# Kernel optimization log

Measured on AMD Instinct MI355X. Metric: run time of the kernel, lower is better.

The kernel has to match this reference:

```python
import jax, jax.numpy as jnp
import numpy as np

N = 100000      # nodes
E = 1600000     # edges
F = 92          # raw node feature length
H = 128         # element_embedding == hidden_encoding (GatedGraphConv out_channels)
STEPS = 6       # mpnn_steps
G = 256         # graphs in batch


def setup_inputs() -> dict:
    key = jax.random.key(0)
    ks = jax.random.split(key, 10)
    s = 0.05
    x = jax.random.normal(ks[0], (N, F), dtype=jnp.float32)
    edge_index = jax.random.randint(ks[1], (2, E), 0, N, dtype=jnp.int64)
    batch = jnp.sort(jax.random.randint(ks[2], (N,), 0, G, dtype=jnp.int64))
    # atom_input: Linear(F, H, bias=False); applied as x @ W_embed with W_embed [F, H]
    W_embed = jax.random.normal(ks[3], (F, H), dtype=jnp.float32) * s
    # GatedGraphConv weight: [num_layers, H, H], used as h @ W_mpnn[i]
    W_mpnn = jax.random.normal(ks[4], (STEPS, H, H), dtype=jnp.float32) * s
    # torch.nn.GRUCell params: weight_ih/hh [3H, H], bias_ih/hh [3H]
    w_ih = jax.random.normal(ks[5], (3 * H, H), dtype=jnp.float32) * s
    w_hh = jax.random.normal(ks[6], (3 * H, H), dtype=jnp.float32) * s
    b_ih = jax.random.normal(ks[7], (3 * H,), dtype=jnp.float32) * s
    b_hh = jax.random.normal(ks[8], (3 * H,), dtype=jnp.float32) * s
    # prediction_layer: Linear(H, 1)
    w_pred = jax.random.normal(ks[9], (H, 1), dtype=jnp.float32) * s
    b_pred = jnp.zeros((1,), dtype=jnp.float32)
    return {"x": x, "edge_index": edge_index, "batch": batch,
            "W_embed": W_embed, "W_mpnn": W_mpnn,
            "w_ih": w_ih, "w_hh": w_hh, "b_ih": b_ih, "b_hh": b_hh,
            "w_pred": w_pred, "b_pred": b_pred}


def reference(x, edge_index, batch, W_embed, W_mpnn, w_ih, w_hh, b_ih, b_hh, w_pred, b_pred):
    n = x.shape[0]
    src, dst = edge_index[0], edge_index[1]  # PyG: messages flow source -> target
    # atom_input (no bias) + tanh; element_embedding == H so no zero-padding needed
    h = jnp.tanh(x @ W_embed)  # [N, H]

    def step(h, W):
        m = h @ W                                             # per-step linear [N, H]
        agg = jax.ops.segment_sum(m[src], dst, num_segments=n)  # scatter-add aggr
        # torch GRUCell(input=agg, hidden=h)
        gi = agg @ w_ih.T + b_ih                              # [N, 3H]
        gh = h @ w_hh.T + b_hh                                # [N, 3H]
        i_r, i_z, i_n = jnp.split(gi, 3, axis=-1)
        h_r, h_z, h_n = jnp.split(gh, 3, axis=-1)
        r = jax.nn.sigmoid(i_r + h_r)
        z = jax.nn.sigmoid(i_z + h_z)
        cand = jnp.tanh(i_n + r * h_n)
        h_new = (1.0 - z) * cand + z * h
        return h_new, None

    h, _ = jax.lax.scan(step, h, W_mpnn)

    # global_mean_pool over graph ids
    sums = jax.ops.segment_sum(h, batch, num_segments=G)                           # [G, H]
    counts = jax.ops.segment_sum(jnp.ones((n, 1), h.dtype), batch, num_segments=G)  # [G, 1]
    pooled = sums / jnp.maximum(counts, 1.0)
    pooled = jax.nn.relu(pooled)
    return (pooled @ w_pred + b_pred)[:, 0]  # [G]
```

## Files before the change

### kernel.cpp

```cpp
#include <hip/hip_runtime.h>
#include <math.h>

#define N_NODES 100000
#define N_PAD   100032
#define N_EDGES 1600000
#define F_IN    92
#define H_DIM   128
#define STEPS   6
#define G_GRAPHS 256
#define TH3     384
#define SSTR    136
#define HSTR    132
#define FPASS   8
#define FRANGE  12500
#define EIDX_CAP 1024

typedef __attribute__((ext_vector_type(8))) short bf16x8;
typedef __attribute__((ext_vector_type(4))) float f32x4;

__device__ __forceinline__ unsigned short f2bf(float x) {
    unsigned u = __float_as_uint(x);
    return (unsigned short)((u + 0x7fffu + ((u >> 16) & 1u)) >> 16);
}
__device__ __forceinline__ float bf2f(unsigned short h) {
    return __uint_as_float(((unsigned)h) << 16);
}

__global__ void fuse_w_kernel(const float* __restrict__ Wm, const float* __restrict__ w_ih,
                              float* __restrict__ M2) {
    int ij = blockIdx.x;
    int i  = ij / TH3;
    int j  = ij - i * TH3;
    int k  = threadIdx.x;
    __shared__ float wj[H_DIM];
    wj[k] = w_ih[j * H_DIM + k];
    __syncthreads();
    const float* wr = Wm + ((size_t)i * H_DIM + k) * H_DIM;
    float acc = 0.f;
    #pragma unroll 4
    for (int c = 0; c < H_DIM; ++c) acc = fmaf(wj[c], wr[c], acc);
    M2[((size_t)i * TH3 + j) * H_DIM + k] = acc;
}

__global__ void pack_kernel(const float* __restrict__ M6, const float* __restrict__ w_hh,
                            unsigned short* __restrict__ PBhi, unsigned short* __restrict__ PBlo) {
    int b    = blockIdx.x;
    int lane = threadIdx.x;
    int kc   = b & 3;
    int ct   = (b >> 2) & 7;
    int mg   = b >> 5;
    int g    = mg % 3;
    int mat  = mg / 3;
    int j    = g * 128 + ct * 16 + (lane & 15);
    int k0   = kc * 32 + (lane >> 4) * 8;
    size_t outBase = ((size_t)b * 64 + lane) * 8;
    #pragma unroll
    for (int jj = 0; jj < 8; ++jj) {
        int k = k0 + jj;
        float v = (mat < 6) ? M6[((size_t)mat * TH3 + j) * H_DIM + k]
                            : w_hh[(size_t)j * H_DIM + k];
        unsigned short hv = f2bf(v);
        PBhi[outBase + jj] = hv;
        PBlo[outBase + jj] = f2bf(v - bf2f(hv));
    }
}

#define ET 16
__global__ void embed_kernel(const float* __restrict__ x, const float* __restrict__ We,
                             unsigned short* __restrict__ h_hi, unsigned short* __restrict__ h_lo) {
    int n0 = blockIdx.x * ET;
    int j  = threadIdx.x;
    __shared__ float xs[ET * F_IN];
    for (int i = j; i < ET * F_IN; i += H_DIM) xs[i] = x[n0 * F_IN + i];
    __syncthreads();
    float acc[ET];
    #pragma unroll
    for (int n = 0; n < ET; ++n) acc[n] = 0.f;
    const float4* xs4 = (const float4*)xs;
    for (int k4 = 0; k4 < F_IN / 4; ++k4) {
        int k = k4 * 4;
        float w0 = We[(k + 0) * H_DIM + j];
        float w1 = We[(k + 1) * H_DIM + j];
        float w2 = We[(k + 2) * H_DIM + j];
        float w3 = We[(k + 3) * H_DIM + j];
        #pragma unroll
        for (int n = 0; n < ET; ++n) {
            float4 a = xs4[n * (F_IN / 4) + k4];
            acc[n] = fmaf(a.x, w0, acc[n]);
            acc[n] = fmaf(a.y, w1, acc[n]);
            acc[n] = fmaf(a.z, w2, acc[n]);
            acc[n] = fmaf(a.w, w3, acc[n]);
        }
    }
    #pragma unroll
    for (int n = 0; n < ET; ++n) {
        float e2 = __expf(2.f * acc[n]);
        float v  = 1.f - 2.f / (e2 + 1.f);
        size_t o = (size_t)(n0 + n) * H_DIM + j;
        unsigned short hv = f2bf(v);
        h_hi[o] = hv;
        h_lo[o] = f2bf(v - bf2f(hv));
    }
}

__global__ void hist_kernel(const int* __restrict__ dst, int* __restrict__ count) {
    int e = blockIdx.x * 256 + threadIdx.x;
    if (e < N_EDGES) atomicAdd(&count[dst[e]], 1);
}

__global__ void scan_block_kernel(const int* __restrict__ count, int* __restrict__ offs,
                                  int* __restrict__ blockSums) {
    __shared__ int tmp[256];
    int i = blockIdx.x * 256 + threadIdx.x;
    int t = threadIdx.x;
    int v = (i < N_NODES) ? count[i] : 0;
    tmp[t] = v;
    __syncthreads();
    for (int d = 1; d < 256; d <<= 1) {
        int add = (t >= d) ? tmp[t - d] : 0;
        __syncthreads();
        tmp[t] += add;
        __syncthreads();
    }
    if (i < N_NODES) offs[i] = tmp[t] - v;
    if (t == 255) blockSums[blockIdx.x] = tmp[255];
}

__global__ void scan_sums_kernel(int* __restrict__ blockSums, int nb) {
    __shared__ int tmp[512];
    int t = threadIdx.x;
    int v = (t < nb) ? blockSums[t] : 0;
    tmp[t] = v;
    __syncthreads();
    for (int d = 1; d < 512; d <<= 1) {
        int add = (t >= d) ? tmp[t - d] : 0;
        __syncthreads();
        tmp[t] += add;
        __syncthreads();
    }
    if (t < nb) blockSums[t] = tmp[t] - v;
}

__global__ void scan_add_kernel(int* __restrict__ offs, const int* __restrict__ blockSums) {
    int i = blockIdx.x * 256 + threadIdx.x;
    if (i < N_NODES) offs[i] += blockSums[blockIdx.x];
    if (i == 0) offs[N_NODES] = N_EDGES;
}

__global__ void fill_kernel(const int* __restrict__ src, const int* __restrict__ dst,
                            const int* __restrict__ offs, int* __restrict__ cursor,
                            int* __restrict__ srcSorted) {
    int e = blockIdx.x * 256 + threadIdx.x;
    if (e >= N_EDGES) return;
    for (int p = 0; p < FPASS; ++p) {
        int lo = p * FRANGE;
        int d = dst[e];
        if (d >= lo && d < lo + FRANGE) {
            int pos = atomicAdd(&cursor[d], 1);
            srcSorted[offs[d] + pos] = src[e];
        }
    }
}

__global__ __launch_bounds__(512, 4) void gru_fused_kernel(
    const unsigned short* __restrict__ h_hi_in,
    unsigned short* __restrict__ h_hi_out,
    unsigned short* __restrict__ h_lo,
    const int* __restrict__ offs, const int* __restrict__ srcS,
    const unsigned short* __restrict__ PBhi, const unsigned short* __restrict__ PBlo,
    int matI, const float* __restrict__ b_ih, const float* __restrict__ b_hh)
{
    __shared__ __align__(16) unsigned short buf[3 * 32 * SSTR];
    __shared__ int eIdx[EIDX_CAP];
    unsigned short* sHh = buf;
    unsigned short* sHl = buf + 32 * SSTR;
    unsigned short* sS  = buf + 2 * 32 * SSTR;
    float* hnF = (float*)buf;

    int nt = blockIdx.x;
    int rowBase = nt * 32;
    int t = threadIdx.x;
    int row = t >> 4;
    int node = rowBase + row;

    int beg = 0, end = 0;
    if (node < N_NODES) { beg = offs[node]; end = offs[node + 1]; }
    int eBegBlk = offs[rowBase < N_NODES ? rowBase : N_NODES];
    int eEndBlk = offs[(rowBase + 32) < N_NODES ? (rowBase + 32) : N_NODES];
    int eCnt = eEndBlk - eBegBlk;

    {
        int c8 = (t & 15) * 8;
        size_t g = (size_t)node * H_DIM + c8;
        int l = row * SSTR + c8;
        *(bf16x8*)&sHh[l] = *(const bf16x8*)(h_hi_in + g);
        *(bf16x8*)&sHl[l] = *(const bf16x8*)(h_lo + g);
    }
    {
        int lim = eCnt < EIDX_CAP ? eCnt : EIDX_CAP;
        for (int k = t; k < lim; k += 512) eIdx[k] = srcS[eBegBlk + k];
    }
    __syncthreads();

    {
        int sub   = t & 15;
        int halfI = sub >> 3;
        int cOff  = (sub & 7) * 16;
        float a[16];
        #pragma unroll
        for (int j = 0; j < 16; ++j) a[j] = 0.f;
        if (node < N_NODES) {
            int len = end - beg;
            int h0  = (len + 1) >> 1;
            int lo  = beg + (halfI ? h0 : 0);
            int hi  = halfI ? end : beg + h0;
            const unsigned short* hb = h_hi_in + cOff;

            auto gatherRun = [&](auto IDXF) {
                int i = lo;
                int n0 = 0, n1 = 0, n2 = 0, n3 = 0;
                bool have4 = (i + 4 <= hi);
                if (have4) { n0 = IDXF(i); n1 = IDXF(i+1); n2 = IDXF(i+2); n3 = IDXF(i+3); }
                while (have4) {
                    const bf16x8* p0 = (const bf16x8*)(hb + (size_t)n0 * H_DIM);
                    const bf16x8* p1 = (const bf16x8*)(hb + (size_t)n1 * H_DIM);
                    const bf16x8* p2 = (const bf16x8*)(hb + (size_t)n2 * H_DIM);
                    const bf16x8* p3 = (const bf16x8*)(hb + (size_t)n3 * H_DIM);
                    bf16x8 v0a = p0[0], v0b = p0[1];
                    bf16x8 v1a = p1[0], v1b = p1[1];
                    bf16x8 v2a = p2[0], v2b = p2[1];
                    bf16x8 v3a = p3[0], v3b = p3[1];
                    i += 4;
                    have4 = (i + 4 <= hi);
                    if (have4) { n0 = IDXF(i); n1 = IDXF(i+1); n2 = IDXF(i+2); n3 = IDXF(i+3); }
                    #pragma unroll
                    for (int j = 0; j < 8; ++j) {
                        a[j]     += (bf2f((unsigned short)v0a[j]) + bf2f((unsigned short)v1a[j]))
                                  + (bf2f((unsigned short)v2a[j]) + bf2f((unsigned short)v3a[j]));
                        a[8 + j] += (bf2f((unsigned short)v0b[j]) + bf2f((unsigned short)v1b[j]))
                                  + (bf2f((unsigned short)v2b[j]) + bf2f((unsigned short)v3b[j]));
                    }
                }
                if (i + 2 <= hi) {
                    int q0 = IDXF(i), q1 = IDXF(i + 1);
                    const bf16x8* p0 = (const bf16x8*)(hb + (size_t)q0 * H_DIM);
                    const bf16x8* p1 = (const bf16x8*)(hb + (size_t)q1 * H_DIM);
                    bf16x8 v0a = p0[0], v0b = p0[1];
                    bf16x8 v1a = p1[0], v1b = p1[1];
                    #pragma unroll
                    for (int j = 0; j < 8; ++j) {
                        a[j]     += bf2f((unsigned short)v0a[j]) + bf2f((unsigned short)v1a[j]);
                        a[8 + j] += bf2f((unsigned short)v0b[j]) + bf2f((unsigned short)v1b[j]);
                    }
                    i += 2;
                }
                if (i < hi) {
                    int q0 = IDXF(i);
                    const bf16x8* p = (const bf16x8*)(hb + (size_t)q0 * H_DIM);
                    bf16x8 va = p[0], vb = p[1];
                    #pragma unroll
                    for (int j = 0; j < 8; ++j) {
                        a[j]     += bf2f((unsigned short)va[j]);
                        a[8 + j] += bf2f((unsigned short)vb[j]);
                    }
                }
            };

            if (eCnt <= EIDX_CAP) {
                int eb = eBegBlk;
                gatherRun([&](int x) { return eIdx[x - eb]; });
            } else {
                gatherRun([&](int x) { return srcS[x]; });
            }
        }
        #pragma unroll
        for (int j = 0; j < 16; ++j) a[j] += __shfl_xor(a[j], 8);
        bf16x8 o;
        #pragma unroll
        for (int j = 0; j < 8; ++j) o[j] = (short)f2bf(a[halfI * 8 + j]);
        *(bf16x8*)&sS[row * SSTR + cOff + halfI * 8] = o;
    }

    int lane = t & 63;
    int ct   = t >> 6;
    int rloc = lane & 15;
    int kOff = (lane >> 4) * 8;

    f32x4 accRZ[2][2], accIn[2], accHn[2];
    #pragma unroll
    for (int rs = 0; rs < 2; ++rs) {
        accRZ[0][rs] = (f32x4){0.f, 0.f, 0.f, 0.f};
        accRZ[1][rs] = (f32x4){0.f, 0.f, 0.f, 0.f};
        accIn[rs]    = (f32x4){0.f, 0.f, 0.f, 0.f};
        accHn[rs]    = (f32x4){0.f, 0.f, 0.f, 0.f};
    }

    for (int kc = 0; kc < 4; ++kc) {
        int aOff = kc * 32 + kOff;
        bf16x8 aHh4[2], aHl4[2];
        #pragma unroll
        for (int rs = 0; rs < 2; ++rs) {
            int al = (rs * 16 + rloc) * SSTR + aOff;
            aHh4[rs] = *(const bf16x8*)(&sHh[al]);
            aHl4[rs] = *(const bf16x8*)(&sHl[al]);
        }
        #pragma unroll
        for (int g = 0; g < 3; ++g) {
            size_t oH = ((size_t)((18 + g) * 32 + ct * 4 + kc) * 64 + lane) * 8;
            bf16x8 bHh = *(const bf16x8*)(PBhi + oH);
            bf16x8 bHl = *(const bf16x8*)(PBlo + oH);
            #pragma unroll
            for (int rs = 0; rs < 2; ++rs) {
                f32x4* tH = (g == 0) ? &accRZ[0][rs] : (g == 1) ? &accRZ[1][rs] : &accHn[rs];
                *tH = __builtin_amdgcn_mfma_f32_16x16x32_bf16(aHh4[rs], bHh, *tH, 0, 0, 0);
                *tH = __builtin_amdgcn_mfma_f32_16x16x32_bf16(aHl4[rs], bHh, *tH, 0, 0, 0);
                *tH = __builtin_amdgcn_mfma_f32_16x16x32_bf16(aHh4[rs], bHl, *tH, 0, 0, 0);
            }
        }
    }

    __syncthreads();

    const int fI0 = matI * 3;
    for (int kc = 0; kc < 4; ++kc) {
        int aOff = kc * 32 + kOff;
        bf16x8 aS[2];
        #pragma unroll
        for (int rs = 0; rs < 2; ++rs)
            aS[rs] = *(const bf16x8*)(&sS[(rs * 16 + rloc) * SSTR + aOff]);
        #pragma unroll
        for (int g = 0; g < 3; ++g) {
            size_t oI = ((size_t)((fI0 + g) * 32 + ct * 4 + kc) * 64 + lane) * 8;
            bf16x8 bIh = *(const bf16x8*)(PBhi + oI);
            bf16x8 bIl = *(const bf16x8*)(PBlo + oI);
            #pragma unroll
            for (int rs = 0; rs < 2; ++rs) {
                f32x4* tI = (g == 0) ? &accRZ[0][rs] : (g == 1) ? &accRZ[1][rs] : &accIn[rs];
                *tI = __builtin_amdgcn_mfma_f32_16x16x32_bf16(aS[rs], bIh, *tI, 0, 0, 0);
                *tI = __builtin_amdgcn_mfma_f32_16x16x32_bf16(aS[rs], bIl, *tI, 0, 0, 0);
            }
        }
    }

    int c = ct * 16 + rloc;
    float br  = b_ih[c] + b_hh[c];
    float bz  = b_ih[128 + c] + b_hh[128 + c];
    float bin = b_ih[256 + c], bhn = b_hh[256 + c];
    int rl = (lane >> 4) * 4;

    float hnv[2][4];
    #pragma unroll
    for (int rs = 0; rs < 2; ++rs) {
        #pragma unroll
        for (int r = 0; r < 4; ++r) {
            int lrow = rs * 16 + rl + r;
            float hold = bf2f(sHh[lrow * SSTR + c]) + bf2f(sHl[lrow * SSTR + c]);
            float rr = 1.f / (1.f + __expf(-(accRZ[0][rs][r] + br)));
            float zz = 1.f / (1.f + __expf(-(accRZ[1][rs][r] + bz)));
            float pre = (accIn[rs][r] + bin) + rr * (accHn[rs][r] + bhn);
            float e2 = __expf(2.f * pre);
            float cand = 1.f - 2.f / (e2 + 1.f);
            hnv[rs][r] = (1.f - zz) * cand + zz * hold;
        }
    }
    __syncthreads();
    #pragma unroll
    for (int rs = 0; rs < 2; ++rs)
        #pragma unroll
        for (int r = 0; r < 4; ++r)
            hnF[(rs * 16 + rl + r) * HSTR + c] = hnv[rs][r];
    __syncthreads();
    #pragma unroll
    for (int i = t; i < 32 * 32; i += 512) {
        int rw = i >> 5;
        int c4 = (i & 31) * 4;
        int gRow = rowBase + rw;
        if (gRow < N_NODES) {
            float4 v = *(const float4*)(&hnF[rw * HSTR + c4]);
            ushort4 hh, ll;
            hh.x = f2bf(v.x); ll.x = f2bf(v.x - bf2f(hh.x));
            hh.y = f2bf(v.y); ll.y = f2bf(v.y - bf2f(hh.y));
            hh.z = f2bf(v.z); ll.z = f2bf(v.z - bf2f(hh.z));
            hh.w = f2bf(v.w); ll.w = f2bf(v.w - bf2f(hh.w));
            size_t o = (size_t)gRow * H_DIM + c4;
            *(ushort4*)(h_hi_out + o) = hh;
            *(ushort4*)(h_lo + o) = ll;
        }
    }
}

__global__ void pool_partial(const unsigned short* __restrict__ h_hi,
                             const unsigned short* __restrict__ h_lo,
                             const int* __restrict__ batch,
                             float* __restrict__ pooled) {
    int b = blockIdx.x;
    int t = threadIdx.x;
    int n0 = b * 64;
    if (n0 >= N_NODES) return;
    int nEnd = n0 + 64 < N_NODES ? n0 + 64 : N_NODES;
    int curG = batch[n0];
    float acc = 0.f;
    for (int n = n0; n < nEnd; ++n) {
        int g = batch[n];
        if (g != curG) {
            atomicAdd(&pooled[curG * H_DIM + t], acc);
            acc = 0.f;
            curG = g;
        }
        size_t o = (size_t)n * H_DIM + t;
        acc += bf2f(h_hi[o]) + bf2f(h_lo[o]);
    }
    atomicAdd(&pooled[curG * H_DIM + t], acc);
}

__global__ void pool_head(const float* __restrict__ pooled, const int* __restrict__ batch,
                          const float* __restrict__ w_pred, const float* __restrict__ b_pred,
                          float* __restrict__ out) {
    int g = blockIdx.x;
    int t = threadIdx.x;
    __shared__ int bounds[2];
    __shared__ float red[2];
    if (t < 2) {
        int target = g + t;
        int lo = 0, hi = N_NODES;
        while (lo < hi) {
            int mid = (lo + hi) >> 1;
            if (batch[mid] < target) lo = mid + 1; else hi = mid;
        }
        bounds[t] = lo;
    }
    __syncthreads();
    int cnt = bounds[1] - bounds[0];
    float pv = pooled[g * H_DIM + t] / fmaxf((float)cnt, 1.f);
    pv = fmaxf(pv, 0.f);
    float v = pv * w_pred[t];
    #pragma unroll
    for (int off = 32; off > 0; off >>= 1) v += __shfl_down(v, off);
    if ((t & 63) == 0) red[t >> 6] = v;
    __syncthreads();
    if (t == 0) out[g] = red[0] + red[1] + b_pred[0];
}

extern "C" void kernel_launch(void* const* d_in, const int* in_sizes, int n_in,
                              void* d_out, int out_size, void* d_ws, size_t ws_size,
                              hipStream_t stream) {
    const float* x      = (const float*)d_in[0];
    const int*   ei     = (const int*)d_in[1];
    const int*   batch  = (const int*)d_in[2];
    const float* We     = (const float*)d_in[3];
    const float* Wm     = (const float*)d_in[4];
    const float* w_ih   = (const float*)d_in[5];
    const float* w_hh   = (const float*)d_in[6];
    const float* b_ih   = (const float*)d_in[7];
    const float* b_hh   = (const float*)d_in[8];
    const float* w_pred = (const float*)d_in[9];
    const float* b_pred = (const float*)d_in[10];
    float* out = (float*)d_out;

    const size_t HN = (size_t)N_PAD * H_DIM;
    unsigned short* h_hiA = (unsigned short*)d_ws;
    unsigned short* h_lo  = h_hiA + HN;
    unsigned short* h_hiB = h_lo + HN;
    float* M6 = (float*)(h_hiB + HN);
    unsigned short* PBhi = (unsigned short*)(M6 + (size_t)STEPS * TH3 * H_DIM);
    unsigned short* PBlo = PBhi + 21 * 32 * 64 * 8;
    int* offs      = (int*)(PBlo + 21 * 32 * 64 * 8);
    int* srcSorted = offs + (N_NODES + 1);
    float* pooled  = (float*)(srcSorted + N_EDGES);
    int* count     = (int*)h_hiB;
    int* cursor    = count + N_NODES;
    int* blockSums = cursor + N_NODES;

    const int* esrc = ei;
    const int* edst = ei + N_EDGES;
    const int EB = (N_EDGES + 255) / 256;
    const int NB = (N_NODES + 255) / 256;

    hipMemsetAsync(count, 0, 2 * (size_t)N_NODES * sizeof(int), stream);
    hipMemsetAsync(pooled, 0, (size_t)G_GRAPHS * H_DIM * sizeof(float), stream);
    hist_kernel<<<EB, 256, 0, stream>>>(edst, count);
    scan_block_kernel<<<NB, 256, 0, stream>>>(count, offs, blockSums);
    scan_sums_kernel<<<1, 512, 0, stream>>>(blockSums, NB);
    scan_add_kernel<<<NB, 256, 0, stream>>>(offs, blockSums);
    fill_kernel<<<EB, 256, 0, stream>>>(esrc, edst, offs, cursor, srcSorted);

    fuse_w_kernel<<<STEPS * TH3, H_DIM, 0, stream>>>(Wm, w_ih, M6);
    pack_kernel<<<21 * 32, 64, 0, stream>>>(M6, w_hh, PBhi, PBlo);
    embed_kernel<<<N_NODES / ET, H_DIM, 0, stream>>>(x, We, h_hiA, h_lo);

    for (int i = 0; i < STEPS; ++i) {
        const unsigned short* hin = (i & 1) ? h_hiB : h_hiA;
        unsigned short*       hout = (i & 1) ? h_hiA : h_hiB;
        gru_fused_kernel<<<N_PAD / 32, 512, 0, stream>>>(hin, hout, h_lo,
                                                         offs, srcSorted, PBhi, PBlo,
                                                         i, b_ih, b_hh);
    }

    pool_partial<<<(N_NODES + 63) / 64, H_DIM, 0, stream>>>(h_hiA, h_lo, batch, pooled);
    pool_head<<<G_GRAPHS, H_DIM, 0, stream>>>(pooled, batch, w_pred, b_pred, out);
}
```

Before: 1.045 ms.

## Tile fuse_w over output rows and alternate gather/MFMA order across blocks

The weight-fusion kernel now has each block compute eight output rows at once, loading w_ih rows into shared memory and reading Wm with float4 loads. This cuts the block count and reuses each Wm row load. In the GRU step kernel, the neighbour gather and the hidden-state MFMA phase become lambdas whose order flips based on a thread/block-derived parity. The aim is to mix memory-bound and compute-bound wavefronts on a CU so they overlap better. The catch is extra register pressure from keeping the accumulators live across the gather, and the gathered sS is only consumed after the barrier.

```diff
diff --git a/kernel.cpp b/kernel.cpp
--- a/kernel.cpp
+++ b/kernel.cpp
@@ -14,6 +14,7 @@
 #define FPASS   8
 #define FRANGE  12500
 #define EIDX_CAP 1024
+#define JT      8
 
 typedef __attribute__((ext_vector_type(8))) short bf16x8;
 typedef __attribute__((ext_vector_type(4))) float f32x4;
@@ -29,17 +30,33 @@
 __global__ void fuse_w_kernel(const float* __restrict__ Wm, const float* __restrict__ w_ih,
                               float* __restrict__ M2) {
     int ij = blockIdx.x;
-    int i  = ij / TH3;
-    int j  = ij - i * TH3;
+    int i  = ij / (TH3 / JT);
+    int j0 = (ij % (TH3 / JT)) * JT;
     int k  = threadIdx.x;
-    __shared__ float wj[H_DIM];
-    wj[k] = w_ih[j * H_DIM + k];
-    __syncthreads();
-    const float* wr = Wm + ((size_t)i * H_DIM + k) * H_DIM;
-    float acc = 0.f;
-    #pragma unroll 4
-    for (int c = 0; c < H_DIM; ++c) acc = fmaf(wj[c], wr[c], acc);
-    M2[((size_t)i * TH3 + j) * H_DIM + k] = acc;
+    __shared__ float wj[JT][H_DIM];
+    for (int idx = k; idx < JT * H_DIM; idx += H_DIM) {
+        int jj = idx >> 7, c = idx & 127;
+        wj[jj][c] = w_ih[(size_t)(j0 + jj) * H_DIM + c];
+    }
+    __syncthreads();
+    const float4* wr4 = (const float4*)(Wm + ((size_t)i * H_DIM + k) * H_DIM);
+    float acc[JT];
+    #pragma unroll
+    for (int jj = 0; jj < JT; ++jj) acc[jj] = 0.f;
+    for (int c4 = 0; c4 < H_DIM / 4; ++c4) {
+        float4 wv = wr4[c4];
+        int c = c4 * 4;
+        #pragma unroll
+        for (int jj = 0; jj < JT; ++jj) {
+            acc[jj] = fmaf(wj[jj][c + 0], wv.x, acc[jj]);
+            acc[jj] = fmaf(wj[jj][c + 1], wv.y, acc[jj]);
+            acc[jj] = fmaf(wj[jj][c + 2], wv.z, acc[jj]);
+            acc[jj] = fmaf(wj[jj][c + 3], wv.w, acc[jj]);
+        }
+    }
+    #pragma unroll
+    for (int jj = 0; jj < JT; ++jj)
+        M2[((size_t)i * TH3 + j0 + jj) * H_DIM + k] = acc[jj];
 }
 
 __global__ void pack_kernel(const float* __restrict__ M6, const float* __restrict__ w_hh,
@@ -202,7 +219,21 @@
     }
     __syncthreads();
 
-    {
+    int lane = t & 63;
+    int ct   = t >> 6;
+    int rloc = lane & 15;
+    int kOff = (lane >> 4) * 8;
+
+    f32x4 accRZ[2][2], accIn[2], accHn[2];
+    #pragma unroll
+    for (int rs = 0; rs < 2; ++rs) {
+        accRZ[0][rs] = (f32x4){0.f, 0.f, 0.f, 0.f};
+        accRZ[1][rs] = (f32x4){0.f, 0.f, 0.f, 0.f};
+        accIn[rs]    = (f32x4){0.f, 0.f, 0.f, 0.f};
+        accHn[rs]    = (f32x4){0.f, 0.f, 0.f, 0.f};
+    }
+
+    auto do_gather = [&]() {
         int sub   = t & 15;
         int halfI = sub >> 3;
         int cOff  = (sub & 7) * 16;
@@ -279,45 +310,36 @@
         #pragma unroll
         for (int j = 0; j < 8; ++j) o[j] = (short)f2bf(a[halfI * 8 + j]);
         *(bf16x8*)&sS[row * SSTR + cOff + halfI * 8] = o;
-    }
-
-    int lane = t & 63;
-    int ct   = t >> 6;
-    int rloc = lane & 15;
-    int kOff = (lane >> 4) * 8;
-
-    f32x4 accRZ[2][2], accIn[2], accHn[2];
-    #pragma unroll
-    for (int rs = 0; rs < 2; ++rs) {
-        accRZ[0][rs] = (f32x4){0.f, 0.f, 0.f, 0.f};
-        accRZ[1][rs] = (f32x4){0.f, 0.f, 0.f, 0.f};
-        accIn[rs]    = (f32x4){0.f, 0.f, 0.f, 0.f};
-        accHn[rs]    = (f32x4){0.f, 0.f, 0.f, 0.f};
-    }
-
-    for (int kc = 0; kc < 4; ++kc) {
-        int aOff = kc * 32 + kOff;
-        bf16x8 aHh4[2], aHl4[2];
-        #pragma unroll
-        for (int rs = 0; rs < 2; ++rs) {
-            int al = (rs * 16 + rloc) * SSTR + aOff;
-            aHh4[rs] = *(const bf16x8*)(&sHh[al]);
-            aHl4[rs] = *(const bf16x8*)(&sHl[al]);
-        }
-        #pragma unroll
-        for (int g = 0; g < 3; ++g) {
-            size_t oH = ((size_t)((18 + g) * 32 + ct * 4 + kc) * 64 + lane) * 8;
-            bf16x8 bHh = *(const bf16x8*)(PBhi + oH);
-            bf16x8 bHl = *(const bf16x8*)(PBlo + oH);
+    };
+
+    auto do_hmfma = [&]() {
+        for (int kc = 0; kc < 4; ++kc) {
+            int aOff = kc * 32 + kOff;
+            bf16x8 aHh4[2], aHl4[2];
             #pragma unroll
             for (int rs = 0; rs < 2; ++rs) {
-                f32x4* tH = (g == 0) ? &accRZ[0][rs] : (g == 1) ? &accRZ[1][rs] : &accHn[rs];
-                *tH = __builtin_amdgcn_mfma_f32_16x16x32_bf16(aHh4[rs], bHh, *tH, 0, 0, 0);
-                *tH = __builtin_amdgcn_mfma_f32_16x16x32_bf16(aHl4[rs], bHh, *tH, 0, 0, 0);
-                *tH = __builtin_amdgcn_mfma_f32_16x16x32_bf16(aHh4[rs], bHl, *tH, 0, 0, 0);
+                int al = (rs * 16 + rloc) * SSTR + aOff;
+                aHh4[rs] = *(const bf16x8*)(&sHh[al]);
+                aHl4[rs] = *(const bf16x8*)(&sHl[al]);
             }
-        }
-    }
+            #pragma unroll
+            for (int g = 0; g < 3; ++g) {
+                size_t oH = ((size_t)((18 + g) * 32 + ct * 4 + kc) * 64 + lane) * 8;
+                bf16x8 bHh = *(const bf16x8*)(PBhi + oH);
+                bf16x8 bHl = *(const bf16x8*)(PBlo + oH);
+                #pragma unroll
+                for (int rs = 0; rs < 2; ++rs) {
+                    f32x4* tH = (g == 0) ? &accRZ[0][rs] : (g == 1) ? &accRZ[1][rs] : &accHn[rs];
+                    *tH = __builtin_amdgcn_mfma_f32_16x16x32_bf16(aHh4[rs], bHh, *tH, 0, 0, 0);
+                    *tH = __builtin_amdgcn_mfma_f32_16x16x32_bf16(aHl4[rs], bHh, *tH, 0, 0, 0);
+                    *tH = __builtin_amdgcn_mfma_f32_16x16x32_bf16(aHh4[rs], bHl, *tH, 0, 0, 0);
+                }
+            }
+        }
+    };
+
+    if ((nt ^ (nt >> 8)) & 1) { do_hmfma(); do_gather(); }
+    else                      { do_gather(); do_hmfma(); }
 
     __syncthreads();
 
@@ -484,7 +506,7 @@
     scan_add_kernel<<<NB, 256, 0, stream>>>(offs, blockSums);
     fill_kernel<<<EB, 256, 0, stream>>>(esrc, edst, offs, cursor, srcSorted);
 
-    fuse_w_kernel<<<STEPS * TH3, H_DIM, 0, stream>>>(Wm, w_ih, M6);
+    fuse_w_kernel<<<STEPS * (TH3 / JT), H_DIM, 0, stream>>>(Wm, w_ih, M6);
     pack_kernel<<<21 * 32, 64, 0, stream>>>(M6, w_hh, PBhi, PBlo);
     embed_kernel<<<N_NODES / ET, H_DIM, 0, stream>>>(x, We, h_hiA, h_lo);
 
```

Result: slower. 1.268 ms (+21.3%).
